# Kernel tuning notes

Measured on AMD Instinct MI355X. Metric: run time of the kernel, lower is better.

The kernel has to match this reference:

```python
import jax, jax.numpy as jnp
import numpy as np

D = 1024      # in_features
H = 8         # heads per branch (head_num // 2)
DH = (D // 2) // H  # 64
OUT = 1024

def _split_heads(x, B, S):
    # [B, S, D/2] -> [B, H, S, DH]
    return x.reshape(B, S, H, DH).transpose(0, 2, 1, 3)

def _attn(q, k, v):
    # q,k,v: [B, H, S, DH]
    scores = jnp.einsum('bhqd,bhkd->bhqk', q, k) / jnp.sqrt(jnp.float32(DH))
    a = jax.nn.softmax(scores, axis=-1)
    return jnp.einsum('bhqk,bhkd->bhqd', a, v)

def setup_inputs() -> dict:
    key = jax.random.key(0)
    ks = jax.random.split(key, 16)
    B, S = 2, 2048
    d2 = D // 2
    sc = lambda fan_in: 1.0 / np.sqrt(fan_in)
    inp = {
        'f1': jax.random.normal(ks[0], (B, S, D), jnp.float32),
        'f2': jax.random.normal(ks[1], (B, S, D), jnp.float32),
    }
    names = ['qs', 'ks', 'vs', 'qc', 'kc', 'vc']
    for i, n in enumerate(names):
        inp['W' + n] = jax.random.uniform(ks[2 + i], (d2, D), jnp.float32, -sc(D), sc(D))
        inp['b' + n] = jax.random.uniform(ks[8 + i], (d2,), jnp.float32, -sc(D), sc(D))
    inp['Wo'] = jax.random.uniform(ks[14], (OUT, 2 * D), jnp.float32, -sc(2 * D), sc(2 * D))
    inp['bo'] = jax.random.uniform(ks[15], (OUT,), jnp.float32, -sc(2 * D), sc(2 * D))
    return inp

def reference(f1, f2, Wqs, bqs, Wks, bks, Wvs, bvs, Wqc, bqc, Wkc, bkc, Wvc, bvc, Wo, bo):
    B, S, _ = f1.shape
    lin = lambda x, W, b: jax.nn.relu(x @ W.T + b)
    qs = lin(f1, Wqs, bqs); ks_ = lin(f1, Wks, bks); vs = lin(f1, Wvs, bvs)
    qc = lin(f1, Wqc, bqc); kc = lin(f2, Wkc, bkc); vc = lin(f2, Wvc, bvc)
    ys = _attn(_split_heads(qs, B, S), _split_heads(ks_, B, S), _split_heads(vs, B, S))
    yc = _attn(_split_heads(qc, B, S), _split_heads(kc, B, S), _split_heads(vc, B, S))
    merge = lambda y: y.transpose(0, 2, 1, 3).reshape(B, S, D // 2)
    # reshape_to_batches followed by reshape_from_batches on vs/vc is identity
    y = jnp.concatenate([merge(ys), merge(yc), vs, vc], axis=-1)  # [B, S, 2D]
    return jax.nn.relu(y @ Wo.T + bo)
```

## Files before the change

kernel.cpp:

```cpp
#include <hip/hip_runtime.h>
#include <hip/hip_bf16.h>

using bf16 = __hip_bfloat16;
typedef __attribute__((ext_vector_type(8))) short bf16x8;
typedef __attribute__((ext_vector_type(4))) float f32x4;

#define MTOT 4096

__device__ __forceinline__ f32x4 fzero() {
    f32x4 z = {0.f, 0.f, 0.f, 0.f};
    return z;
}

__device__ __forceinline__ f32x4 mfma16(bf16x8 a, bf16x8 b, f32x4 c) {
    return __builtin_amdgcn_mfma_f32_16x16x32_bf16(a, b, c, 0, 0, 0);
}

typedef const __attribute__((address_space(1))) unsigned int* gas_ptr;
typedef __attribute__((address_space(3))) unsigned int* las_ptr;
__device__ __forceinline__ void async_copy16(const bf16* g, bf16* l) {
    __builtin_amdgcn_global_load_lds((gas_ptr)(const void*)g, (las_ptr)(void*)l, 16, 0, 0);
}

__device__ __forceinline__ bf16x8 load8(const bf16* p) {
    return *(const bf16x8*)p;
}
__device__ __forceinline__ bf16x8 load8(const float* p) {
    float4 a = *(const float4*)p;
    float4 b = *(const float4*)(p + 4);
    bf16 t[8];
    t[0] = __float2bfloat16(a.x); t[1] = __float2bfloat16(a.y);
    t[2] = __float2bfloat16(a.z); t[3] = __float2bfloat16(a.w);
    t[4] = __float2bfloat16(b.x); t[5] = __float2bfloat16(b.y);
    t[6] = __float2bfloat16(b.z); t[7] = __float2bfloat16(b.w);
    return *(const bf16x8*)t;
}

__device__ __forceinline__ void store_out(bf16* C, size_t idx, float v) {
    C[idx] = __float2bfloat16(v);
}
__device__ __forceinline__ void store_out(float* C, size_t idx, float v) {
    C[idx] = v;
}

__global__ void MultiHeadSelfCrossAttention_7834020348638_kernel(float* out, int n) {
    int i = blockIdx.x * blockDim.x + threadIdx.x;
    if (i < n) out[i] = 0.25f;
}

struct CvtArgs {
    const float* src[9];
    bf16* dst[9];
    int n8[9];
};
__global__ void cvt_kernel(CvtArgs a) {
    int seg = blockIdx.y;
    int t = blockIdx.x * blockDim.x + threadIdx.x;
    if (t < a.n8[seg])
        *(bf16x8*)(a.dst[seg] + (size_t)t * 8) = load8(a.src[seg] + (size_t)t * 8);
}

template <int BN, typename TC>
__device__ __forceinline__ void gemm_fast(
    const bf16* __restrict__ A, int lda,
    const bf16* __restrict__ Bt, int ldb,
    const float* __restrict__ bias,
    TC* __restrict__ C, int ldc,
    int K, int m0, int n0)
{
    constexpr int NI  = BN / 32;
    constexpr int ACH = 128 * 64 / 8 / 256;
    constexpr int BCH = BN * 64 / 8 / 256;

    __shared__ bf16 As[128 * 64];
    __shared__ bf16 Bs[BN * 64];

    const int tid  = threadIdx.x;
    const int lane = tid & 63;
    const int l15  = lane & 15, quad = lane >> 4;
    const int wave = tid >> 6;
    const int wr   = wave >> 1, wc = wave & 1;

    f32x4 acc[4][NI];
#pragma unroll
    for (int mi = 0; mi < 4; mi++)
#pragma unroll
        for (int ni = 0; ni < NI; ni++)
            acc[mi][ni] = fzero();

    for (int k0 = 0; k0 < K; k0 += 64) {
        __syncthreads();
#pragma unroll
        for (int i = 0; i < ACH; i++) {
            int idx = i * 256 + tid;
            int r   = idx >> 3;
            int cg  = (idx & 7) * 8;
            async_copy16(A + (size_t)(m0 + r) * lda + k0 + cg, &As[idx * 8]);
        }
#pragma unroll
        for (int i = 0; i < BCH; i++) {
            int idx = i * 256 + tid;
            int r   = idx >> 3;
            int cg  = (idx & 7) * 8;
            async_copy16(Bt + (size_t)(n0 + r) * ldb + k0 + cg, &Bs[idx * 8]);
        }
        __syncthreads();

#pragma unroll
        for (int ks = 0; ks < 2; ks++) {
            bf16x8 af[4], bfr[NI];
#pragma unroll
            for (int mi = 0; mi < 4; mi++)
                af[mi] = *(const bf16x8*)&As[(wr * 64 + mi * 16 + l15) * 64 + ks * 32 + quad * 8];
#pragma unroll
            for (int ni = 0; ni < NI; ni++)
                bfr[ni] = *(const bf16x8*)&Bs[(wc * (BN / 2) + ni * 16 + l15) * 64 + ks * 32 + quad * 8];
#pragma unroll
            for (int mi = 0; mi < 4; mi++)
#pragma unroll
                for (int ni = 0; ni < NI; ni++)
                    acc[mi][ni] = mfma16(af[mi], bfr[ni], acc[mi][ni]);
        }
    }

#pragma unroll
    for (int ni = 0; ni < NI; ni++) {
        int col = n0 + wc * (BN / 2) + ni * 16 + l15;
        float bb = bias[col];
#pragma unroll
        for (int mi = 0; mi < 4; mi++) {
#pragma unroll
            for (int r = 0; r < 4; r++) {
                int row = m0 + wr * 64 + mi * 16 + quad * 4 + r;
                store_out(C, (size_t)row * ldc + col, fmaxf(acc[mi][ni][r] + bb, 0.f));
            }
        }
    }
}

template <int BN, typename TA, typename TB, typename TC>
__device__ __forceinline__ void gemm_reg(
    const TA* __restrict__ A, int lda,
    const TB* __restrict__ Bt, int ldb,
    const float* __restrict__ bias,
    TC* __restrict__ C, int ldc,
    int K, int m0, int n0)
{
    constexpr int NI  = BN / 32;
    constexpr int BCH = BN * 4 / 256;

    __shared__ bf16 As[128 * 32];
    __shared__ bf16 Bs[BN * 32];

    const int tid  = threadIdx.x;
    const int lane = tid & 63;
    const int l15  = lane & 15, quad = lane >> 4;
    const int wave = tid >> 6;
    const int wr   = wave >> 1, wc = wave & 1;

    f32x4 acc[4][NI];
#pragma unroll
    for (int mi = 0; mi < 4; mi++)
#pragma unroll
        for (int ni = 0; ni < NI; ni++)
            acc[mi][ni] = fzero();

    for (int k0 = 0; k0 < K; k0 += 32) {
        bf16x8 ra[2], rb[BCH];
#pragma unroll
        for (int i = 0; i < 2; i++) {
            int idx = i * 256 + tid;
            ra[i] = load8(A + (size_t)(m0 + (idx >> 2)) * lda + k0 + (idx & 3) * 8);
        }
#pragma unroll
        for (int i = 0; i < BCH; i++) {
            int idx = i * 256 + tid;
            rb[i] = load8(Bt + (size_t)(n0 + (idx >> 2)) * ldb + k0 + (idx & 3) * 8);
        }
        __syncthreads();
#pragma unroll
        for (int i = 0; i < 2; i++)
            *(bf16x8*)&As[(i * 256 + tid) * 8] = ra[i];
#pragma unroll
        for (int i = 0; i < BCH; i++)
            *(bf16x8*)&Bs[(i * 256 + tid) * 8] = rb[i];
        __syncthreads();

        bf16x8 af[4], bfr[NI];
#pragma unroll
        for (int mi = 0; mi < 4; mi++)
            af[mi] = *(const bf16x8*)&As[(wr * 64 + mi * 16 + l15) * 32 + quad * 8];
#pragma unroll
        for (int ni = 0; ni < NI; ni++)
            bfr[ni] = *(const bf16x8*)&Bs[(wc * (BN / 2) + ni * 16 + l15) * 32 + quad * 8];
#pragma unroll
        for (int mi = 0; mi < 4; mi++)
#pragma unroll
            for (int ni = 0; ni < NI; ni++)
                acc[mi][ni] = mfma16(af[mi], bfr[ni], acc[mi][ni]);
    }

#pragma unroll
    for (int ni = 0; ni < NI; ni++) {
        int col = n0 + wc * (BN / 2) + ni * 16 + l15;
        float bb = bias[col];
#pragma unroll
        for (int mi = 0; mi < 4; mi++) {
#pragma unroll
            for (int r = 0; r < 4; r++) {
                int row = m0 + wr * 64 + mi * 16 + quad * 4 + r;
                store_out(C, (size_t)row * ldc + col, fmaxf(acc[mi][ni][r] + bb, 0.f));
            }
        }
    }
}

__global__ void proj_fast(
    const bf16* __restrict__ F1, const bf16* __restrict__ F2,
    const bf16* __restrict__ Wb,
    const float* __restrict__ bqs, const float* __restrict__ bks,
    const float* __restrict__ bvs, const float* __restrict__ bqc,
    const float* __restrict__ bkc, const float* __restrict__ bvc,
    bf16* __restrict__ Y, bf16* Qs, bf16* Ks, bf16* Qc, bf16* Kc)
{
    const int g = blockIdx.z;
    const bf16* X; const float* bi; bf16* C; int ldc;
    switch (g) {
        case 0:  X = F1; bi = bqs; C = Qs;       ldc = 512;  break;
        case 1:  X = F1; bi = bks; C = Ks;       ldc = 512;  break;
        case 2:  X = F1; bi = bvs; C = Y + 1024; ldc = 2048; break;
        case 3:  X = F1; bi = bqc; C = Qc;       ldc = 512;  break;
        case 4:  X = F2; bi = bkc; C = Kc;       ldc = 512;  break;
        default: X = F2; bi = bvc; C = Y + 1536; ldc = 2048; break;
    }
    gemm_fast<128, bf16>(X, 1024, Wb + (size_t)g * 512 * 1024, 1024, bi, C, ldc,
                         1024, blockIdx.y * 128, blockIdx.x * 128);
}

__global__ void out_fast(const bf16* __restrict__ Y, const bf16* __restrict__ WoB,
                         const float* __restrict__ bo, float* __restrict__ out)
{
    gemm_fast<64, float>(Y, 2048, WoB, 2048, bo, out, 1024, 2048,
                         blockIdx.y * 128, blockIdx.x * 64);
}

__global__ void proj_reg(
    const float* __restrict__ f1, const float* __restrict__ f2,
    const float* __restrict__ Wqs, const float* __restrict__ bqs,
    const float* __restrict__ Wks, const float* __restrict__ bks,
    const float* __restrict__ Wvs, const float* __restrict__ bvs,
    const float* __restrict__ Wqc, const float* __restrict__ bqc,
    const float* __restrict__ Wkc, const float* __restrict__ bkc,
    const float* __restrict__ Wvc, const float* __restrict__ bvc,
    bf16* __restrict__ Y, bf16* Qs, bf16* Ks, bf16* Qc, bf16* Kc)
{
    const int g = blockIdx.z;
    const float *X, *W, *bi; bf16* C; int ldc;
    switch (g) {
        case 0:  X = f1; W = Wqs; bi = bqs; C = Qs;       ldc = 512;  break;
        case 1:  X = f1; W = Wks; bi = bks; C = Ks;       ldc = 512;  break;
        case 2:  X = f1; W = Wvs; bi = bvs; C = Y + 1024; ldc = 2048; break;
        case 3:  X = f1; W = Wqc; bi = bqc; C = Qc;       ldc = 512;  break;
        case 4:  X = f2; W = Wkc; bi = bkc; C = Kc;       ldc = 512;  break;
        default: X = f2; W = Wvc; bi = bvc; C = Y + 1536; ldc = 2048; break;
    }
    gemm_reg<128>(X, 1024, W, 1024, bi, C, ldc, 1024, blockIdx.y * 128, blockIdx.x * 128);
}

__global__ void out_reg(const bf16* __restrict__ Y, const float* __restrict__ Wo,
                        const float* __restrict__ bo, float* __restrict__ out)
{
    gemm_reg<64>(Y, 2048, Wo, 2048, bo, out, 1024, 2048, blockIdx.y * 128, blockIdx.x * 64);
}

__global__ __launch_bounds__(256, 4) void attn_kernel(
    const bf16* __restrict__ Qsb, const bf16* __restrict__ Ksb,
    const bf16* __restrict__ Qcb, const bf16* __restrict__ Kcb,
    bf16* __restrict__ Y)
{
    __shared__ bf16 QP[64 * 72];
    __shared__ bf16 Ksh[64 * 72];
    __shared__ bf16 Vsh[64 * 72];

    const int tid  = threadIdx.x;
    const int lane = tid & 63;
    const int l15  = lane & 15, quad = lane >> 4;
    const int wave = tid >> 6;
    const int qt = blockIdx.x, bh = blockIdx.y, br = blockIdx.z;
    const int b = bh >> 3, h = bh & 7;

    const bf16* Qb = (br ? Qcb : Qsb) + (size_t)b * 2048 * 512 + h * 64;
    const bf16* Kb = (br ? Kcb : Ksb) + (size_t)b * 2048 * 512 + h * 64;
    const bf16* Vb = Y + (size_t)b * 2048 * 2048 + 1024 + br * 512 + h * 64;
    bf16*       Ob = Y + (size_t)b * 2048 * 2048 +        br * 512 + h * 64;
    const int q0 = qt * 64;

#pragma unroll
    for (int i = 0; i < 2; i++) {
        int idx = i * 256 + tid;
        int r = idx >> 3, c0 = (idx & 7) * 8;
        *(bf16x8*)&QP[r * 72 + c0] = *(const bf16x8*)&Qb[(size_t)(q0 + r) * 512 + c0];
    }
    __syncthreads();

    bf16x8 qf[2];
#pragma unroll
    for (int ks = 0; ks < 2; ks++)
        qf[ks] = *(const bf16x8*)&QP[(wave * 16 + l15) * 72 + ks * 32 + quad * 8];

    const short one_bits = l15 == 0 ? (short)0x3F80 : (short)0;
    bf16x8 onesf;
#pragma unroll
    for (int j = 0; j < 8; j++) onesf[j] = one_bits;

    f32x4 o[4], o_l;
    o_l = fzero();
#pragma unroll
    for (int ni = 0; ni < 4; ni++) o[ni] = fzero();

    const int kr0 = tid >> 3, kc0 = (tid & 7) * 8;
    const int kr1 = (256 + tid) >> 3;

    bf16x8 kr[2], vr[2];
    kr[0] = *(const bf16x8*)&Kb[(size_t)kr0 * 512 + kc0];
    kr[1] = *(const bf16x8*)&Kb[(size_t)kr1 * 512 + kc0];
    vr[0] = *(const bf16x8*)&Vb[(size_t)lane * 2048 + (0 * 4 + wave) * 8];
    vr[1] = *(const bf16x8*)&Vb[(size_t)lane * 2048 + (1 * 4 + wave) * 8];

    for (int jt = 0; jt < 32; jt++) {
        __syncthreads();
        *(bf16x8*)&Ksh[kr0 * 72 + kc0] = kr[0];
        *(bf16x8*)&Ksh[kr1 * 72 + kc0] = kr[1];
#pragma unroll
        for (int i = 0; i < 2; i++) {
            int cg = i * 4 + wave;
            const bf16* e = (const bf16*)&vr[i];
#pragma unroll
            for (int j = 0; j < 8; j++)
                Vsh[(cg * 8 + j) * 72 + lane] = e[j];
        }
        __syncthreads();

        {
            const int s0n = (jt < 31) ? (jt + 1) * 64 : 31 * 64;
            kr[0] = *(const bf16x8*)&Kb[(size_t)(s0n + kr0) * 512 + kc0];
            kr[1] = *(const bf16x8*)&Kb[(size_t)(s0n + kr1) * 512 + kc0];
            vr[0] = *(const bf16x8*)&Vb[(size_t)(s0n + lane) * 2048 + (0 * 4 + wave) * 8];
            vr[1] = *(const bf16x8*)&Vb[(size_t)(s0n + lane) * 2048 + (1 * 4 + wave) * 8];
        }

        f32x4 s[4];
#pragma unroll
        for (int ni = 0; ni < 4; ni++) s[ni] = fzero();
#pragma unroll
        for (int ni = 0; ni < 4; ni++)
#pragma unroll
            for (int ks = 0; ks < 2; ks++) {
                bf16x8 kf = *(const bf16x8*)&Ksh[(ni * 16 + l15) * 72 + ks * 32 + quad * 8];
                s[ni] = mfma16(qf[ks], kf, s[ni]);
            }

#pragma unroll
        for (int ni = 0; ni < 4; ni++)
#pragma unroll
            for (int r = 0; r < 4; r++) {
                float p = __expf(s[ni][r] * 0.125f - 4.0f);
                QP[(wave * 16 + quad * 4 + r) * 72 + ni * 16 + l15] = __float2bfloat16(p);
            }

#pragma unroll
        for (int ks = 0; ks < 2; ks++) {
            bf16x8 pf = *(const bf16x8*)&QP[(wave * 16 + l15) * 72 + ks * 32 + quad * 8];
#pragma unroll
            for (int ni = 0; ni < 4; ni++) {
                bf16x8 vf = *(const bf16x8*)&Vsh[(ni * 16 + l15) * 72 + ks * 32 + quad * 8];
                o[ni] = mfma16(pf, vf, o[ni]);
            }
            o_l = mfma16(pf, onesf, o_l);
        }
    }

#pragma unroll
    for (int r = 0; r < 4; r++) {
        float lsum = __shfl(o_l[r], quad << 4);
        float inv = 1.f / lsum;
        int row = q0 + wave * 16 + quad * 4 + r;
#pragma unroll
        for (int ni = 0; ni < 4; ni++)
            Ob[(size_t)row * 2048 + ni * 16 + l15] = __float2bfloat16(o[ni][r] * inv);
    }
}

extern "C" void kernel_launch(void* const* d_in, const int* in_sizes, int n_in,
                              void* d_out, int out_size, void* d_ws, size_t ws_size,
                              hipStream_t stream) {
    const size_t out_bytes = (size_t)out_size * sizeof(float);
    const size_t ws_base = ((size_t)MTOT * 2048 + 4 * (size_t)MTOT * 512) * 2;
    const size_t ws_fast = ws_base + ((size_t)2 * MTOT * 1024 + 6 * 512 * 1024 + 1024 * 2048) * 2;

    if (n_in != 16) { hipMemsetAsync(d_out, 0x43, out_bytes, stream); return; }
    if (ws_size < ws_base) { hipMemsetAsync(d_out, 0x41, out_bytes, stream); return; }

    const float* f1  = (const float*)d_in[0];
    const float* f2  = (const float*)d_in[1];
    const float* Wqs = (const float*)d_in[2];  const float* bqs = (const float*)d_in[3];
    const float* Wks = (const float*)d_in[4];  const float* bks = (const float*)d_in[5];
    const float* Wvs = (const float*)d_in[6];  const float* bvs = (const float*)d_in[7];
    const float* Wqc = (const float*)d_in[8];  const float* bqc = (const float*)d_in[9];
    const float* Wkc = (const float*)d_in[10]; const float* bkc = (const float*)d_in[11];
    const float* Wvc = (const float*)d_in[12]; const float* bvc = (const float*)d_in[13];
    const float* Wo  = (const float*)d_in[14]; const float* bo  = (const float*)d_in[15];

    bf16* Y  = (bf16*)d_ws;
    bf16* Qs = Y  + (size_t)MTOT * 2048;
    bf16* Ks = Qs + (size_t)MTOT * 512;
    bf16* Qc = Ks + (size_t)MTOT * 512;
    bf16* Kc = Qc + (size_t)MTOT * 512;
    float* out = (float*)d_out;

    if (ws_size >= ws_fast) {
        bf16* F1  = Kc + (size_t)MTOT * 512;
        bf16* F2  = F1 + (size_t)MTOT * 1024;
        bf16* Wb  = F2 + (size_t)MTOT * 1024;
        bf16* WoB = Wb + (size_t)6 * 512 * 1024;

        CvtArgs ca;
        ca.src[0] = f1;  ca.dst[0] = F1;  ca.n8[0] = MTOT * 1024 / 8;
        ca.src[1] = f2;  ca.dst[1] = F2;  ca.n8[1] = MTOT * 1024 / 8;
        const float* ws_[6] = {Wqs, Wks, Wvs, Wqc, Wkc, Wvc};
        for (int i = 0; i < 6; i++) {
            ca.src[2 + i] = ws_[i];
            ca.dst[2 + i] = Wb + (size_t)i * 512 * 1024;
            ca.n8[2 + i]  = 512 * 1024 / 8;
        }
        ca.src[8] = Wo; ca.dst[8] = WoB; ca.n8[8] = 1024 * 2048 / 8;

        cvt_kernel<<<dim3((MTOT * 1024 / 8 + 255) / 256, 9), 256, 0, stream>>>(ca);
        proj_fast<<<dim3(4, 32, 6), 256, 0, stream>>>(
            F1, F2, Wb, bqs, bks, bvs, bqc, bkc, bvc, Y, Qs, Ks, Qc, Kc);
        attn_kernel<<<dim3(32, 16, 2), 256, 0, stream>>>(Qs, Ks, Qc, Kc, Y);
        out_fast<<<dim3(16, 32), 256, 0, stream>>>(Y, WoB, bo, out);
    } else {
        proj_reg<<<dim3(4, 32, 6), 256, 0, stream>>>(
            f1, f2, Wqs, bqs, Wks, bks, Wvs, bvs, Wqc, bqc, Wkc, bkc, Wvc, bvc,
            Y, Qs, Ks, Qc, Kc);
        attn_kernel<<<dim3(32, 16, 2), 256, 0, stream>>>(Qs, Ks, Qc, Kc, Y);
        out_reg<<<dim3(16, 32), 256, 0, stream>>>(Y, Wo, bo, out);
    }
}
```

Measured before the change: 264.3 us.

## Pre-transpose V and keep softmax probabilities in registers via transposed MFMA

Adds a separate kernel that writes V in a transposed [head, dim, seq] layout, so the attention kernel can store V tiles into shared memory with plain vector stores instead of scalar transposing writes. The attention kernel now computes S^T with 16x16x16 MFMAs, which lets the exp'd probabilities be fed straight from registers as the A operand of the PV MFMA. This removes the shared-memory round trip for P and the Q staging buffer. Row sums are gathered in registers with shuffles rather than an extra ones-vector MFMA. The cost is an extra kernel launch and an extra global pass over V, plus the narrower K=16 MFMA instruction.

```diff
diff --git a/kernel.cpp b/kernel.cpp
--- a/kernel.cpp
+++ b/kernel.cpp
@@ -2,6 +2,7 @@
 #include <hip/hip_bf16.h>
 
 using bf16 = __hip_bfloat16;
+typedef __attribute__((ext_vector_type(4))) short bf16x4;
 typedef __attribute__((ext_vector_type(8))) short bf16x8;
 typedef __attribute__((ext_vector_type(4))) float f32x4;
 
@@ -14,6 +15,9 @@
 
 __device__ __forceinline__ f32x4 mfma16(bf16x8 a, bf16x8 b, f32x4 c) {
     return __builtin_amdgcn_mfma_f32_16x16x32_bf16(a, b, c, 0, 0, 0);
+}
+__device__ __forceinline__ f32x4 mfma1k(bf16x4 a, bf16x4 b, f32x4 c) {
+    return __builtin_amdgcn_mfma_f32_16x16x16bf16_1k(a, b, c, 0, 0, 0);
 }
 
 typedef const __attribute__((address_space(1))) unsigned int* gas_ptr;
@@ -60,6 +64,32 @@
         *(bf16x8*)(a.dst[seg] + (size_t)t * 8) = load8(a.src[seg] + (size_t)t * 8);
 }
 
+__global__ void vtrans_kernel(const bf16* __restrict__ Y, bf16* __restrict__ Vt) {
+    __shared__ bf16 T[64 * 72];
+    const int tid = threadIdx.x;
+    const int s0 = blockIdx.x * 64, bh = blockIdx.y, br = blockIdx.z;
+    const int b = bh >> 3, h = bh & 7;
+    const bf16* src = Y + (size_t)b * 2048 * 2048 + 1024 + br * 512 + h * 64;
+    bf16* dst = Vt + (size_t)((br * 2 + b) * 8 + h) * 64 * 2048;
+
+#pragma unroll
+    for (int i = 0; i < 2; i++) {
+        int idx = i * 256 + tid;
+        int sl = idx >> 3, c0 = (idx & 7) * 8;
+        *(bf16x8*)&T[sl * 72 + c0] = *(const bf16x8*)&src[(size_t)(s0 + sl) * 2048 + c0];
+    }
+    __syncthreads();
+#pragma unroll
+    for (int i = 0; i < 2; i++) {
+        int idx = i * 256 + tid;
+        int dl = idx >> 3, sc = (idx & 7) * 8;
+        bf16 e[8];
+#pragma unroll
+        for (int j = 0; j < 8; j++) e[j] = T[(sc + j) * 72 + dl];
+        *(bf16x8*)&dst[(size_t)dl * 2048 + s0 + sc] = *(const bf16x8*)e;
+    }
+}
+
 template <int BN, typename TC>
 __device__ __forceinline__ void gemm_fast(
     const bf16* __restrict__ A, int lda,
@@ -276,9 +306,8 @@
 __global__ __launch_bounds__(256, 4) void attn_kernel(
     const bf16* __restrict__ Qsb, const bf16* __restrict__ Ksb,
     const bf16* __restrict__ Qcb, const bf16* __restrict__ Kcb,
-    bf16* __restrict__ Y)
-{
-    __shared__ bf16 QP[64 * 72];
+    const bf16* __restrict__ Vt, bf16* __restrict__ Y)
+{
     __shared__ bf16 Ksh[64 * 72];
     __shared__ bf16 Vsh[64 * 72];
 
@@ -289,105 +318,89 @@
     const int qt = blockIdx.x, bh = blockIdx.y, br = blockIdx.z;
     const int b = bh >> 3, h = bh & 7;
 
-    const bf16* Qb = (br ? Qcb : Qsb) + (size_t)b * 2048 * 512 + h * 64;
-    const bf16* Kb = (br ? Kcb : Ksb) + (size_t)b * 2048 * 512 + h * 64;
-    const bf16* Vb = Y + (size_t)b * 2048 * 2048 + 1024 + br * 512 + h * 64;
-    bf16*       Ob = Y + (size_t)b * 2048 * 2048 +        br * 512 + h * 64;
+    const bf16* Qb  = (br ? Qcb : Qsb) + (size_t)b * 2048 * 512 + h * 64;
+    const bf16* Kb  = (br ? Kcb : Ksb) + (size_t)b * 2048 * 512 + h * 64;
+    const bf16* VtB = Vt + (size_t)((br * 2 + b) * 8 + h) * 64 * 2048;
+    bf16*       Ob  = Y + (size_t)b * 2048 * 2048 + br * 512 + h * 64;
     const int q0 = qt * 64;
 
-#pragma unroll
-    for (int i = 0; i < 2; i++) {
-        int idx = i * 256 + tid;
-        int r = idx >> 3, c0 = (idx & 7) * 8;
-        *(bf16x8*)&QP[r * 72 + c0] = *(const bf16x8*)&Qb[(size_t)(q0 + r) * 512 + c0];
-    }
-    __syncthreads();
-
-    bf16x8 qf[2];
-#pragma unroll
-    for (int ks = 0; ks < 2; ks++)
-        qf[ks] = *(const bf16x8*)&QP[(wave * 16 + l15) * 72 + ks * 32 + quad * 8];
-
-    const short one_bits = l15 == 0 ? (short)0x3F80 : (short)0;
-    bf16x8 onesf;
-#pragma unroll
-    for (int j = 0; j < 8; j++) onesf[j] = one_bits;
-
-    f32x4 o[4], o_l;
-    o_l = fzero();
-#pragma unroll
-    for (int ni = 0; ni < 4; ni++) o[ni] = fzero();
-
-    const int kr0 = tid >> 3, kc0 = (tid & 7) * 8;
-    const int kr1 = (256 + tid) >> 3;
+    bf16x4 qf[4];
+#pragma unroll
+    for (int kd = 0; kd < 4; kd++)
+        qf[kd] = *(const bf16x4*)&Qb[(size_t)(q0 + wave * 16 + l15) * 512 + kd * 16 + quad * 4];
+
+    f32x4 o[4];
+#pragma unroll
+    for (int dt = 0; dt < 4; dt++) o[dt] = fzero();
+    float rs = 0.f;
+
+    const int r0 = tid >> 3, c0 = (tid & 7) * 8;
+    const int r1 = 32 + r0;
 
     bf16x8 kr[2], vr[2];
-    kr[0] = *(const bf16x8*)&Kb[(size_t)kr0 * 512 + kc0];
-    kr[1] = *(const bf16x8*)&Kb[(size_t)kr1 * 512 + kc0];
-    vr[0] = *(const bf16x8*)&Vb[(size_t)lane * 2048 + (0 * 4 + wave) * 8];
-    vr[1] = *(const bf16x8*)&Vb[(size_t)lane * 2048 + (1 * 4 + wave) * 8];
+    kr[0] = *(const bf16x8*)&Kb[(size_t)r0 * 512 + c0];
+    kr[1] = *(const bf16x8*)&Kb[(size_t)r1 * 512 + c0];
+    vr[0] = *(const bf16x8*)&VtB[(size_t)r0 * 2048 + c0];
+    vr[1] = *(const bf16x8*)&VtB[(size_t)r1 * 2048 + c0];
 
     for (int jt = 0; jt < 32; jt++) {
         __syncthreads();
-        *(bf16x8*)&Ksh[kr0 * 72 + kc0] = kr[0];
-        *(bf16x8*)&Ksh[kr1 * 72 + kc0] = kr[1];
-#pragma unroll
-        for (int i = 0; i < 2; i++) {
-            int cg = i * 4 + wave;
-            const bf16* e = (const bf16*)&vr[i];
-#pragma unroll
-            for (int j = 0; j < 8; j++)
-                Vsh[(cg * 8 + j) * 72 + lane] = e[j];
-        }
+        *(bf16x8*)&Ksh[r0 * 72 + c0] = kr[0];
+        *(bf16x8*)&Ksh[r1 * 72 + c0] = kr[1];
+        *(bf16x8*)&Vsh[r0 * 72 + c0] = vr[0];
+        *(bf16x8*)&Vsh[r1 * 72 + c0] = vr[1];
         __syncthreads();
 
         {
             const int s0n = (jt < 31) ? (jt + 1) * 64 : 31 * 64;
-            kr[0] = *(const bf16x8*)&Kb[(size_t)(s0n + kr0) * 512 + kc0];
-            kr[1] = *(const bf16x8*)&Kb[(size_t)(s0n + kr1) * 512 + kc0];
-            vr[0] = *(const bf16x8*)&Vb[(size_t)(s0n + lane) * 2048 + (0 * 4 + wave) * 8];
-            vr[1] = *(const bf16x8*)&Vb[(size_t)(s0n + lane) * 2048 + (1 * 4 + wave) * 8];
-        }
-
-        f32x4 s[4];
-#pragma unroll
-        for (int ni = 0; ni < 4; ni++) s[ni] = fzero();
-#pragma unroll
-        for (int ni = 0; ni < 4; ni++)
-#pragma unroll
-            for (int ks = 0; ks < 2; ks++) {
-                bf16x8 kf = *(const bf16x8*)&Ksh[(ni * 16 + l15) * 72 + ks * 32 + quad * 8];
-                s[ni] = mfma16(qf[ks], kf, s[ni]);
+            kr[0] = *(const bf16x8*)&Kb[(size_t)(s0n + r0) * 512 + c0];
+            kr[1] = *(const bf16x8*)&Kb[(size_t)(s0n + r1) * 512 + c0];
+            vr[0] = *(const bf16x8*)&VtB[(size_t)r0 * 2048 + s0n + c0];
+            vr[1] = *(const bf16x8*)&VtB[(size_t)r1 * 2048 + s0n + c0];
+        }
+
+        f32x4 st[4];
+#pragma unroll
+        for (int kt = 0; kt < 4; kt++) st[kt] = fzero();
+#pragma unroll
+        for (int kt = 0; kt < 4; kt++)
+#pragma unroll
+            for (int kd = 0; kd < 4; kd++) {
+                bf16x4 kf = *(const bf16x4*)&Ksh[(kt * 16 + l15) * 72 + kd * 16 + quad * 4];
+                st[kt] = mfma1k(kf, qf[kd], st[kt]);
             }
 
-#pragma unroll
-        for (int ni = 0; ni < 4; ni++)
+        bf16x4 pfr[4];
+#pragma unroll
+        for (int kt = 0; kt < 4; kt++) {
 #pragma unroll
             for (int r = 0; r < 4; r++) {
-                float p = __expf(s[ni][r] * 0.125f - 4.0f);
-                QP[(wave * 16 + quad * 4 + r) * 72 + ni * 16 + l15] = __float2bfloat16(p);
+                float p = __expf(st[kt][r] * 0.125f - 4.0f);
+                bf16 pb = __float2bfloat16(p);
+                pfr[kt][r] = *(const short*)&pb;
+                rs += __bfloat162float(pb);
             }
-
-#pragma unroll
-        for (int ks = 0; ks < 2; ks++) {
-            bf16x8 pf = *(const bf16x8*)&QP[(wave * 16 + l15) * 72 + ks * 32 + quad * 8];
-#pragma unroll
-            for (int ni = 0; ni < 4; ni++) {
-                bf16x8 vf = *(const bf16x8*)&Vsh[(ni * 16 + l15) * 72 + ks * 32 + quad * 8];
-                o[ni] = mfma16(pf, vf, o[ni]);
+        }
+
+#pragma unroll
+        for (int dt = 0; dt < 4; dt++)
+#pragma unroll
+            for (int kt = 0; kt < 4; kt++) {
+                bf16x4 vf = *(const bf16x4*)&Vsh[(dt * 16 + l15) * 72 + kt * 16 + quad * 4];
+                o[dt] = mfma1k(pfr[kt], vf, o[dt]);
             }
-            o_l = mfma16(pf, onesf, o_l);
-        }
-    }
+    }
+
+    rs += __shfl_xor(rs, 16);
+    rs += __shfl_xor(rs, 32);
 
 #pragma unroll
     for (int r = 0; r < 4; r++) {
-        float lsum = __shfl(o_l[r], quad << 4);
-        float inv = 1.f / lsum;
+        float inv = 1.f / __shfl(rs, quad * 4 + r);
         int row = q0 + wave * 16 + quad * 4 + r;
 #pragma unroll
-        for (int ni = 0; ni < 4; ni++)
-            Ob[(size_t)row * 2048 + ni * 16 + l15] = __float2bfloat16(o[ni][r] * inv);
+        for (int dt = 0; dt < 4; dt++)
+            Ob[(size_t)row * 2048 + dt * 16 + l15] = __float2bfloat16(o[dt][r] * inv);
     }
 }
 
@@ -395,7 +408,7 @@
                               void* d_out, int out_size, void* d_ws, size_t ws_size,
                               hipStream_t stream) {
     const size_t out_bytes = (size_t)out_size * sizeof(float);
-    const size_t ws_base = ((size_t)MTOT * 2048 + 4 * (size_t)MTOT * 512) * 2;
+    const size_t ws_base = ((size_t)MTOT * 2048 + 4 * (size_t)MTOT * 512 + (size_t)4 * 64 * 2048 * 8) * 2;
     const size_t ws_fast = ws_base + ((size_t)2 * MTOT * 1024 + 6 * 512 * 1024 + 1024 * 2048) * 2;
 
     if (n_in != 16) { hipMemsetAsync(d_out, 0x43, out_bytes, stream); return; }
@@ -416,10 +429,11 @@
     bf16* Ks = Qs + (size_t)MTOT * 512;
     bf16* Qc = Ks + (size_t)MTOT * 512;
     bf16* Kc = Qc + (size_t)MTOT * 512;
+    bf16* Vt = Kc + (size_t)MTOT * 512;
     float* out = (float*)d_out;
 
     if (ws_size >= ws_fast) {
-        bf16* F1  = Kc + (size_t)MTOT * 512;
+        bf16* F1  = Vt + (size_t)4 * 64 * 2048 * 8;
         bf16* F2  = F1 + (size_t)MTOT * 1024;
         bf16* Wb  = F2 + (size_t)MTOT * 1024;
         bf16* WoB = Wb + (size_t)6 * 512 * 1024;
@@ -438,13 +452,15 @@
         cvt_kernel<<<dim3((MTOT * 1024 / 8 + 255) / 256, 9), 256, 0, stream>>>(ca);
         proj_fast<<<dim3(4, 32, 6), 256, 0, stream>>>(
             F1, F2, Wb, bqs, bks, bvs, bqc, bkc, bvc, Y, Qs, Ks, Qc, Kc);
-        attn_kernel<<<dim3(32, 16, 2), 256, 0, stream>>>(Qs, Ks, Qc, Kc, Y);
+        vtrans_kernel<<<dim3(32, 16, 2), 256, 0, stream>>>(Y, Vt);
+        attn_kernel<<<dim3(32, 16, 2), 256, 0, stream>>>(Qs, Ks, Qc, Kc, Vt, Y);
         out_fast<<<dim3(16, 32), 256, 0, stream>>>(Y, WoB, bo, out);
     } else {
         proj_reg<<<dim3(4, 32, 6), 256, 0, stream>>>(
             f1, f2, Wqs, bqs, Wks, bks, Wvs, bvs, Wqc, bqc, Wkc, bkc, Wvc, bvc,
             Y, Qs, Ks, Qc, Kc);
-        attn_kernel<<<dim3(32, 16, 2), 256, 0, stream>>>(Qs, Ks, Qc, Kc, Y);
+        vtrans_kernel<<<dim3(32, 16, 2), 256, 0, stream>>>(Y, Vt);
+        attn_kernel<<<dim3(32, 16, 2), 256, 0, stream>>>(Qs, Ks, Qc, Kc, Vt, Y);
         out_reg<<<dim3(16, 32), 256, 0, stream>>>(Y, Wo, bo, out);
     }
 }
```

Measured after the change: 264.4 us. Within noise of the previous version (+0.0%).
